# Kernel optimization log

Hardware: AMD Instinct MI355X
Metric: run time of the kernel (lower is better)

## Reference

```python
import jax, jax.numpy as jnp
import numpy as np


def _conv2d(x, w, b, dilation=1):
    pad = dilation * (w.shape[-1] // 2)
    y = jax.lax.conv_general_dilated(x, w, (1, 1), [(pad, pad), (pad, pad)],
                                     rhs_dilation=(dilation, dilation),
                                     dimension_numbers=("NCHW", "OIHW", "NCHW"))
    return y + b[None, :, None, None]


def _bn(x, gamma, beta, mean, var):
    # eval-mode BatchNorm2d, eps=1e-5
    inv = gamma / jnp.sqrt(var + 1e-5)
    return (x - mean[None, :, None, None]) * inv[None, :, None, None] + beta[None, :, None, None]


def _frft2d(x, angles):
    # Faithful port of the source frft2d, including the quirk that
    # temp[shft, :] indexes the BATCH dim: since shft is a permutation of
    # 0..N-1, the net effect is that batch entries 0..N-1 get (i)fft'd along
    # axis -2 and entries >= N are untouched.
    temp = jnp.swapaxes(x, -1, -2)
    BC = temp.shape[0]
    for a in angles:
        a = a % 4
        N = temp.shape[-2]
        sN = np.float32(np.sqrt(N))
        mask = (jnp.arange(BC) < N)[:, None, None]
        if a == 1:
            temp = jnp.where(mask, jnp.fft.fft(temp, axis=-2) / sN, temp)
        elif a == 2:
            temp = jnp.flip(temp, axis=-2)
        elif a == 3:
            temp = jnp.where(mask, jnp.fft.ifft(temp, axis=-2) * sN, temp)
        temp = jnp.swapaxes(temp, -1, -2)
    return temp


def setup_inputs() -> dict:
    key = jax.random.key(0)
    ks = jax.random.split(key, 12)
    B, C, H, W = 4, 64, 256, 256
    f = lambda k, shape, s=0.1: jax.random.normal(k, shape, dtype=jnp.float32) * s
    z1 = jnp.zeros((1,), jnp.float32)
    o1 = jnp.ones((1,), jnp.float32)
    return {
        "x": jax.random.normal(ks[0], (B, C, H, W), dtype=jnp.float32),
        "kernel_map": jnp.ones((H, W), dtype=jnp.float32),
        "theta_w": f(ks[1], (1, 1, 3, 3)), "theta_b": z1,
        "phase_w": f(ks[2], (1, 1, 3, 3)), "phase_b": z1,
        "phase_gamma": o1, "phase_beta": z1, "phase_mean": z1, "phase_var": o1,
        "amp_w": f(ks[3], (1, 1, 1, 1)), "amp_b": z1,
        "ms_w1": f(ks[4], (1, 1, 3, 3)), "ms_b1": z1,
        "ms_w2": f(ks[5], (1, 1, 3, 3)), "ms_b2": z1,
        "ms_w3": f(ks[6], (1, 1, 3, 3)), "ms_b3": z1,
        "fc1_w": f(ks[7], (16, 1)), "fc1_b": jnp.zeros((16,), jnp.float32),
        "fc2_w": f(ks[8], (1, 16)), "fc2_b": z1,
        "fin_w": f(ks[9], (1, 6, 1, 1)), "fin_b": z1,
        "fin_gamma": o1, "fin_beta": z1, "fin_mean": z1, "fin_var": o1,
    }


def reference(x, kernel_map, theta_w, theta_b, phase_w, phase_b,
              phase_gamma, phase_beta, phase_mean, phase_var,
              amp_w, amp_b, ms_w1, ms_b1, ms_w2, ms_b2, ms_w3, ms_b3,
              fc1_w, fc1_b, fc2_w, fc2_b, fin_w, fin_b,
              fin_gamma, fin_beta, fin_mean, fin_var):
    B, C, H, W = x.shape
    BC = B * C
    xf = x.reshape(BC, H, W)
    trker = jnp.clip(jax.nn.softplus(kernel_map), 1e-3, 10.0)
    # Riesz kernels, p=(1,1) => sin(pi/2)
    Y = (jnp.arange(H, dtype=jnp.float32) + 1.0)[:, None]
    X = (jnp.arange(W, dtype=jnp.float32) + 1.0)[None, :]
    sa = np.float32(np.sin(0.5 * np.pi))
    denom = jnp.sqrt((X / sa) ** 2 + (Y / sa) ** 2) + 1e-6
    dx = ((-1j) * (X / sa) / denom).astype(jnp.complex64) * trker
    dy = ((-1j) * (Y / sa) / denom).astype(jnp.complex64) * trker
    fa = _frft2d(xf.astype(jnp.complex64), [1, 1])
    R1 = jnp.abs(_frft2d(dx * fa, [-1, -1])) + 1e-6
    R2 = jnp.abs(_frft2d(dy * fa, [-1, -1])) + 1e-6
    A = jnp.sqrt(jax.nn.relu(xf ** 2 + R1 ** 2 + R2 ** 2) + 1e-6)[:, None]
    P = jnp.arctan2(jnp.sqrt(R1 ** 2 + R2 ** 2) + 1e-6, xf + 1e-6)[:, None]
    theta = jnp.arctan2(R2, R1 + 1e-6)[:, None]
    G_theta = theta * jax.nn.sigmoid(_conv2d(theta, theta_w, theta_b))
    P_prime = jax.nn.relu(_bn(_conv2d(P, phase_w, phase_b),
                              phase_gamma, phase_beta, phase_mean, phase_var))
    A_boost = A + jax.nn.relu(_conv2d(A, amp_w, amp_b))
    ms = jnp.concatenate([_conv2d(A_boost, ms_w1, ms_b1, 1),
                          _conv2d(A_boost, ms_w2, ms_b2, 2),
                          _conv2d(A_boost, ms_w3, ms_b3, 3)], axis=1)
    # adaptive_avg_pool2d to (H, W) is the identity here
    gf = jnp.mean(A_boost, axis=(2, 3))  # (BC, 1)
    gw = jax.nn.sigmoid(jax.nn.relu(gf @ fc1_w.T + fc1_b) @ fc2_w.T + fc2_b)
    gw = gw[:, :, None, None]  # (BC,1,1,1)
    fusion = jnp.concatenate([A_boost, P_prime, G_theta, ms * gw], axis=1)  # (BC,6,H,W)
    fused = _bn(_conv2d(fusion, fin_w, fin_b), fin_gamma, fin_beta, fin_mean, fin_var)
    fused = jnp.clip(jax.nn.relu(fused), 0.0, 1.0)
    return fused.reshape(B, C, H, W)
```

## Files before the change

kernel.cpp:

```cpp
#include <hip/hip_runtime.h>
#include <hip/hip_fp16.h>
#include <math.h>

#define PI_F 3.14159265358979323846f
#define ROWB 2112ull
#define IMGB (ROWB * 256ull)

__device__ __forceinline__ unsigned rev8(unsigned v){ return __brev(v) >> 24; }

__device__ __forceinline__ float2 cmulf(float2 a, float2 b){ return make_float2(a.x*b.x - a.y*b.y, a.x*b.y + a.y*b.x); }
__device__ __forceinline__ float2 cmulc(float2 a, float2 b){ return make_float2(a.x*b.x + a.y*b.y, a.y*b.x - a.x*b.y); }
__device__ __forceinline__ float2 cadd (float2 a, float2 b){ return make_float2(a.x+b.x, a.y+b.y); }
__device__ __forceinline__ float2 csub (float2 a, float2 b){ return make_float2(a.x-b.x, a.y-b.y); }
__device__ __forceinline__ float2 eix(float a){ float s, c; __sincosf(a, &s, &c); return make_float2(c, s); }
__device__ __forceinline__ float2 sx(float2 v, int d){ return make_float2(__shfl_xor(v.x, d), __shfl_xor(v.y, d)); }

__device__ __forceinline__ float frcp(float x){ float r; asm("v_rcp_f32 %0, %1" : "=v"(r) : "v"(x)); return r; }

__device__ __forceinline__ float fast_atan2pos(float y, float x){
  const float ax = fabsf(x);
  const float mn = fminf(ax, y), mx = fmaxf(ax, y);
  const float t  = mn * frcp(mx);
  const float z  = t * t;
  float p = -0.01172120f;
  p = fmaf(p, z,  0.05265332f);
  p = fmaf(p, z, -0.11643287f);
  p = fmaf(p, z,  0.19354346f);
  p = fmaf(p, z, -0.33262347f);
  p = fmaf(p, z,  0.99997726f);
  p = p * t;
  p = (y > ax) ? (1.57079632679f - p) : p;
  p = (x < 0.f) ? (3.14159265359f - p) : p;
  return p;
}

__device__ __forceinline__ unsigned packh2u(float a, float b){
  return __builtin_bit_cast(unsigned, __floats2half2_rn(a, b));
}
__device__ __forceinline__ float2 unpackh2(float p){
  return __half22float2(__builtin_bit_cast(__half2, p));
}

struct Twid { float2 w, w2, t[6]; };
__device__ __forceinline__ void mktw(Twid& T, int lane){
  T.w  = eix(-(2.0f * PI_F / 256.0f) * (float)lane);
  T.w2 = cmulf(T.w, T.w);
  #pragma unroll
  for (int st = 0; st < 6; ++st){
    const int d = 32 >> st;
    T.t[st] = eix(-(PI_F / (float)d) * (float)(lane & (d - 1)));
  }
}

__device__ __forceinline__ void fwd_head(float2 v[4], const Twid& T){
  const float2 t0 = cadd(v[0], v[2]);
  const float2 b0 = cmulf(csub(v[0], v[2]), T.w);
  const float2 t1 = cadd(v[1], v[3]);
  const float2 w64 = make_float2(T.w.y, -T.w.x);
  const float2 b1 = cmulf(csub(v[1], v[3]), w64);
  v[0] = cadd(t0, t1);
  v[1] = cmulf(csub(t0, t1), T.w2);
  v[2] = cadd(b0, b1);
  v[3] = cmulf(csub(b0, b1), T.w2);
}
__device__ __forceinline__ void inv_tail(float2 v[4], const Twid& T){
  const float2 uci = make_float2(T.w.y, T.w.x);
  const float2 m1 = cmulc(v[1], T.w2);
  const float2 m3a = cmulc(v[3], T.w2);
  const float2 n0 = cadd(v[0], m1), n1 = csub(v[0], m1);
  const float2 n2 = cadd(v[2], m3a), n3 = csub(v[2], m3a);
  const float2 m2 = cmulc(n2, T.w);
  const float2 m3 = cmulf(n3, uci);
  v[0] = cadd(n0, m2); v[2] = csub(n0, m2);
  v[1] = cadd(n1, m3); v[3] = csub(n1, m3);
}

__device__ __forceinline__ void fft256_fwd_sel(float2 v[4], int lane, const Twid& T){
  fwd_head(v, T);
  #pragma unroll
  for (int st = 0; st < 6; ++st){
    const int d = 32 >> st;
    const float2 tw = T.t[st];
    const bool hi = (lane & d) != 0;
    #pragma unroll
    for (int s = 0; s < 4; ++s){
      const float2 p  = sx(v[s], d);
      const float2 bo = cmulf(csub(p, v[s]), tw);
      const float2 lo = cadd(v[s], p);
      v[s] = hi ? bo : lo;
    }
  }
}
__device__ __forceinline__ void fft256_inv2_sel(float2 a[4], float2 b[4], int lane, const Twid& T){
  #pragma unroll
  for (int st = 0; st < 6; ++st){
    const int d = 1 << st;
    const float2 tw = T.t[5 - st];
    const bool hi = (lane & d) != 0;
    #pragma unroll
    for (int s = 0; s < 4; ++s){
      const float2 pa = sx(a[s], d);
      const float2 pb = sx(b[s], d);
      const float2 ma = cmulc(hi ? a[s] : pa, tw);
      const float2 mb = cmulc(hi ? b[s] : pb, tw);
      a[s] = hi ? csub(pa, ma) : cadd(a[s], ma);
      b[s] = hi ? csub(pb, mb) : cadd(b[s], mb);
    }
  }
  inv_tail(a, T);
  inv_tail(b, T);
}

__device__ __forceinline__ float2 stage_ab(float2 v, float2 p, float Ax, float Ay, float Bx, float By){
  float2 o;
  o.x = v.x*Ax - v.y*Ay + p.x*Bx - p.y*By;
  o.y = v.x*Ay + v.y*Ax + p.x*By + p.y*Bx;
  return o;
}
__device__ __forceinline__ void fft256_fwd2(float2 a[4], float2 b[4], int lane, const Twid& T){
  fwd_head(a, T);
  fwd_head(b, T);
  #pragma unroll
  for (int st = 0; st < 6; ++st){
    const int d = 32 >> st;
    const float2 t = T.t[st];
    const bool hi = (lane & d) != 0;
    const float Ax = hi ? -t.x : 1.f, Ay = hi ? -t.y : 0.f;
    const float Bx = hi ?  t.x : 1.f, By = hi ?  t.y : 0.f;
    #pragma unroll
    for (int s = 0; s < 4; ++s){
      const float2 pa = sx(a[s], d);
      const float2 pb = sx(b[s], d);
      a[s] = stage_ab(a[s], pa, Ax, Ay, Bx, By);
      b[s] = stage_ab(b[s], pb, Ax, Ay, Bx, By);
    }
  }
}
__device__ __forceinline__ void fft256_inv2(float2 a[4], float2 b[4], int lane, const Twid& T){
  #pragma unroll
  for (int st = 0; st < 6; ++st){
    const int d = 1 << st;
    const float2 t = T.t[5 - st];
    const bool hi = (lane & d) != 0;
    const float Ax = hi ? -t.x : 1.f, Ay = hi ?  t.y : 0.f;
    const float Bx = hi ?  1.f : t.x, By = hi ?  0.f : -t.y;
    #pragma unroll
    for (int s = 0; s < 4; ++s){
      const float2 pa = sx(a[s], d);
      const float2 pb = sx(b[s], d);
      a[s] = stage_ab(a[s], pa, Ax, Ay, Bx, By);
      b[s] = stage_ab(b[s], pb, Ax, Ay, Bx, By);
    }
  }
  inv_tail(a, T);
  inv_tail(b, T);
}

__global__ __launch_bounds__(256) void k0_prep(const float* __restrict__ km,
                                               float* __restrict__ sTabS,
                                               float* __restrict__ zrow){
  const int idx = blockIdx.x * 256 + threadIdx.x;
  const int q = idx >> 8, r = idx & 255;
  const int u = rev8(q), v = rev8(r);
  const float kv = km[u * 256 + v];
  float sp = fmaxf(kv, 0.f) + log1pf(expf(-fabsf(kv)));
  sp = fminf(fmaxf(sp, 1e-3f), 10.f);
  const float fu = (float)(u + 1), fv = (float)(v + 1);
  sTabS[idx] = sp / (sqrtf(fu * fu + fv * fv) + 1e-6f) * (1.0f / 65536.0f);
  if (blockIdx.x == 0){
    zrow[threadIdx.x] = 0.f;
    zrow[threadIdx.x + 256] = 0.f;
    if (threadIdx.x < 16) zrow[threadIdx.x + 512] = 0.f;
  }
}

__global__ __launch_bounds__(256) void k1_row(const float* __restrict__ x, char* __restrict__ arena){
  const int grp = threadIdx.x >> 6, lane = threadIdx.x & 63;
  const int rs = blockIdx.x * 8 + grp * 2;
  Twid T; mktw(T, lane);
  const float* xr0 = x + (size_t)rs * 256;
  const float* xr1 = xr0 + 256;
  float2 a[4], b[4];
  #pragma unroll
  for (int s = 0; s < 4; ++s){
    a[s] = make_float2(xr0[lane + 64 * s], 0.f);
    b[s] = make_float2(xr1[lane + 64 * s], 0.f);
  }
  fft256_fwd2(a, b, lane, T);
  float2* S0 = (float2*)(arena + (size_t)rs * ROWB);
  float2* S1 = (float2*)(arena + (size_t)(rs + 1) * ROWB);
  #pragma unroll
  for (int s = 0; s < 4; ++s){ S0[lane + 64 * s] = a[s]; S1[lane + 64 * s] = b[s]; }
}

__global__ __launch_bounds__(512) void k2_col(char* __restrict__ arena, const float* __restrict__ sTabS){
  __shared__ float2 lds[256 * 9];
  const int tid = threadIdx.x;
  const int b  = blockIdx.x >> 5;
  const int u0 = (blockIdx.x & 31) << 3;
  char* base = arena + (size_t)b * IMGB;

  #pragma unroll
  for (int k = 0; k < 4; ++k){
    const int idx = tid + (k << 9);
    const int r = idx >> 3, cc = idx & 7;
    lds[r * 9 + (cc ^ ((r >> 3) & 7))] = *(const float2*)(base + (size_t)r * ROWB + (size_t)(u0 + cc) * 8);
  }
  __syncthreads();

  const int wv = tid >> 6, lane = tid & 63;
  Twid T; mktw(T, lane);
  const int r6 = __brev(lane) >> 26;
  float fvv[4];
  fvv[0] = (float)(4 * r6 + 0 + 1);
  fvv[1] = (float)(4 * r6 + 2 + 1);
  fvv[2] = (float)(4 * r6 + 1 + 1);
  fvv[3] = (float)(4 * r6 + 3 + 1);
  const int swb = (lane >> 3) & 7;

  {
    const int c = wv;
    const int q = u0 + c;
    const int swc = c ^ swb;
    float2 F[4];
    #pragma unroll
    for (int s = 0; s < 4; ++s) F[s] = lds[(lane + 64 * s) * 9 + swc];
    fft256_fwd_sel(F, lane, T);
    float sc[4];
    #pragma unroll
    for (int s = 0; s < 4; ++s) sc[s] = sTabS[q * 256 + lane + 64 * s];
    const float fu = (float)(rev8((unsigned)q) + 1);
    float2 G1[4], G2[4];
    #pragma unroll
    for (int s = 0; s < 4; ++s){
      const float a1 = fvv[s] * sc[s];
      const float a2 = fu * sc[s];
      G1[s] = make_float2(a1 * F[s].y, -a1 * F[s].x);
      G2[s] = make_float2(a2 * F[s].y, -a2 * F[s].x);
    }
    fft256_inv2_sel(G1, G2, lane, T);
    #pragma unroll
    for (int s = 0; s < 4; ++s)
      lds[(lane + 64 * s) * 9 + swc] =
          make_float2(__uint_as_float(packh2u(G1[s].x, G1[s].y)),
                      __uint_as_float(packh2u(G2[s].x, G2[s].y)));
  }
  __syncthreads();
  #pragma unroll
  for (int k = 0; k < 4; ++k){
    const int idx = tid + (k << 9);
    const int r = idx >> 3, cc = idx & 7;
    *(float2*)(base + (size_t)r * ROWB + (size_t)(u0 + cc) * 8) = lds[r * 9 + (cc ^ ((r >> 3) & 7))];
  }
}

__global__ __launch_bounds__(256) void k3_rowinv(const float* __restrict__ x, char* __restrict__ arena,
    const float* __restrict__ ampw, const float* __restrict__ ampb,
    float* __restrict__ rowsum){
  const int grp = threadIdx.x >> 6, lane = threadIdx.x & 63;
  const int rs = blockIdx.x * 4 + grp;
  Twid T; mktw(T, lane);
  char* rowb = arena + (size_t)rs * ROWB;
  float2 g1[4], g2[4];
  #pragma unroll
  for (int s = 0; s < 4; ++s){
    const float2 pk = *(const float2*)(rowb + (size_t)(lane + 64 * s) * 8);
    g1[s] = unpackh2(pk.x); g2[s] = unpackh2(pk.y);
  }
  fft256_inv2(g1, g2, lane, T);
  const float aw = *ampw, ab = *ampb;
  const float* xr = x + (size_t)rs * 256;
  float* Arow = (float*)(rowb + 16);
  unsigned* Prow = (unsigned*)(rowb + 1072);
  float sum = 0.f;
  #pragma unroll
  for (int s = 0; s < 4; ++s){
    const int j = lane + 64 * s;
    const float xv = xr[j];
    const float R1 = sqrtf(fmaf(g1[s].x, g1[s].x, g1[s].y * g1[s].y)) + 1e-6f;
    const float R2 = sqrtf(fmaf(g2[s].x, g2[s].x, g2[s].y * g2[s].y)) + 1e-6f;
    const float rr = fmaf(R1, R1, R2 * R2);
    const float A = sqrtf(fmaxf(fmaf(xv, xv, rr), 0.f) + 1e-6f);
    const float P  = fast_atan2pos(sqrtf(rr) + 1e-6f, xv + 1e-6f);
    const float Th = fast_atan2pos(R2, R1 + 1e-6f);
    const float Ab = A + fmaxf(fmaf(aw, A, ab), 0.f);
    Arow[j] = Ab;
    Prow[j] = packh2u(P, Th);
    sum += Ab;
  }
  #pragma unroll
  for (int off = 32; off; off >>= 1) sum += __shfl_down(sum, off);
  if (lane == 0) rowsum[rs] = sum;
}

__global__ __launch_bounds__(256) void kpad(char* __restrict__ arena){
  char* row = arena + (size_t)blockIdx.x * IMGB + (size_t)threadIdx.x * ROWB;
  const float4 z = make_float4(0.f, 0.f, 0.f, 0.f);
  *(float4*)(row)         = z;
  *(float4*)(row + 1040)  = z;
  *(float4*)(row + 1056)  = z;
  *(float4*)(row + 2096)  = z;
}

__global__ __launch_bounds__(256) void k4_gw(const float* __restrict__ rowsum,
    const float* __restrict__ fc1w, const float* __restrict__ fc1b,
    const float* __restrict__ fc2w, const float* __restrict__ fc2b,
    float* __restrict__ gw){
  __shared__ float red[256];
  const int tid = threadIdx.x;
  red[tid] = rowsum[blockIdx.x * 256 + tid];
  __syncthreads();
  #pragma unroll
  for (int off = 128; off; off >>= 1){
    if (tid < off) red[tid] += red[tid + off];
    __syncthreads();
  }
  if (tid == 0){
    const float gf = red[0] * (1.0f / 65536.0f);
    float acc = fc2b[0];
    #pragma unroll
    for (int k = 0; k < 16; ++k)
      acc += fc2w[k] * fmaxf(gf * fc1w[k] + fc1b[k], 0.f);
    gw[blockIdx.x] = frcp(1.f + __expf(-acc));
  }
}

__global__ __launch_bounds__(256) void k5_fuse(
    const char* __restrict__ arena, const float* __restrict__ zrowf,
    const float* __restrict__ gwp,
    const float* __restrict__ theta_w, const float* __restrict__ theta_b,
    const float* __restrict__ phase_w, const float* __restrict__ phase_b,
    const float* __restrict__ phase_gamma, const float* __restrict__ phase_beta,
    const float* __restrict__ phase_mean, const float* __restrict__ phase_var,
    const float* __restrict__ ms_w1, const float* __restrict__ ms_b1,
    const float* __restrict__ ms_w2, const float* __restrict__ ms_b2,
    const float* __restrict__ ms_w3, const float* __restrict__ ms_b3,
    const float* __restrict__ fin_w, const float* __restrict__ fin_b,
    const float* __restrict__ fin_gamma, const float* __restrict__ fin_beta,
    const float* __restrict__ fin_mean, const float* __restrict__ fin_var,
    float* __restrict__ out){
  const int z = blockIdx.z;
  const int tx = threadIdx.x & 15, ty = threadIdx.x >> 4;
  const int j0 = (blockIdx.x << 6) + (tx << 2);
  const int i0 = (blockIdx.y << 6) + (ty << 2);
  const char* img = arena + (size_t)z * IMGB;

  float tw9[9], pw9[9], w1[9], w2[9], w3[9];
  #pragma unroll
  for (int k = 0; k < 9; ++k){
    tw9[k] = theta_w[k]; pw9[k] = phase_w[k];
    w1[k] = ms_w1[k]; w2[k] = ms_w2[k]; w3[k] = ms_w3[k];
  }
  const float b1s = ms_b1[0], b2s = ms_b2[0], b3s = ms_b3[0];
  const float tbs = theta_b[0], pbs = phase_b[0];

  float4 m1[4], m2[4], m3[4], at[4], ap[4], Ac[4], Tc[4];
  #pragma unroll
  for (int oi = 0; oi < 4; ++oi){
    m1[oi] = make_float4(b1s, b1s, b1s, b1s);
    m2[oi] = make_float4(b2s, b2s, b2s, b2s);
    m3[oi] = make_float4(b3s, b3s, b3s, b3s);
    at[oi] = make_float4(tbs, tbs, tbs, tbs);
    ap[oi] = make_float4(pbs, pbs, pbs, pbs);
  }

  #pragma unroll
  for (int lr = 0; lr < 10; ++lr){
    const int ar = i0 - 3 + lr;
    const float* rowA = ((unsigned)ar < 256u) ? (const float*)(img + (size_t)ar * ROWB) : zrowf;
    const float4 va = *(const float4*)(rowA + j0);
    const float4 vb = *(const float4*)(rowA + j0 + 4);
    const float4 vc = *(const float4*)(rowA + j0 + 8);
    const float a[12] = {va.x, va.y, va.z, va.w, vb.x, vb.y, vb.z, vb.w, vc.x, vc.y, vc.z, vc.w};
    #pragma unroll
    for (int oi = 0; oi < 4; ++oi){
      const int dd = lr - 3 - oi;
      if (dd >= -1 && dd <= 1){
        const int wr = (dd + 1) * 3;
        #pragma unroll
        for (int dx = -1; dx <= 1; ++dx){
          const float w = w1[wr + dx + 1];
          m1[oi].x += w * a[4 + 0 + dx]; m1[oi].y += w * a[4 + 1 + dx];
          m1[oi].z += w * a[4 + 2 + dx]; m1[oi].w += w * a[4 + 3 + dx];
        }
      }
      if (dd == -2 || dd == 0 || dd == 2){
        const int wr = (dd / 2 + 1) * 3;
        #pragma unroll
        for (int dx = -1; dx <= 1; ++dx){
          const float w = w2[wr + dx + 1];
          m2[oi].x += w * a[4 + 0 + 2 * dx]; m2[oi].y += w * a[4 + 1 + 2 * dx];
          m2[oi].z += w * a[4 + 2 + 2 * dx]; m2[oi].w += w * a[4 + 3 + 2 * dx];
        }
      }
      if (dd == -3 || dd == 0 || dd == 3){
        const int wr = (dd / 3 + 1) * 3;
        #pragma unroll
        for (int dx = -1; dx <= 1; ++dx){
          const float w = w3[wr + dx + 1];
          m3[oi].x += w * a[4 + 0 + 3 * dx]; m3[oi].y += w * a[4 + 1 + 3 * dx];
          m3[oi].z += w * a[4 + 2 + 3 * dx]; m3[oi].w += w * a[4 + 3 + 3 * dx];
        }
      }
      if (dd == 0) Ac[oi] = make_float4(a[4], a[5], a[6], a[7]);
    }
  }

  #pragma unroll
  for (int lr = 0; lr < 6; ++lr){
    const int ar = i0 - 1 + lr;
    const unsigned* rowP = ((unsigned)ar < 256u) ? (const unsigned*)(img + (size_t)ar * ROWB + 1056)
                                                 : (const unsigned*)zrowf;
    const uint4 ua = *(const uint4*)(rowP + j0);
    const uint4 ub = *(const uint4*)(rowP + j0 + 4);
    const uint4 uc = *(const uint4*)(rowP + j0 + 8);
    const unsigned uu[12] = {ua.x, ua.y, ua.z, ua.w, ub.x, ub.y, ub.z, ub.w, uc.x, uc.y, uc.z, uc.w};
    float p[12], t[12];
    #pragma unroll
    for (int k = 0; k < 12; ++k){
      const float2 pt = unpackh2(__builtin_bit_cast(float, uu[k]));
      p[k] = pt.x; t[k] = pt.y;
    }
    #pragma unroll
    for (int oi = 0; oi < 4; ++oi){
      const int dd = lr - 1 - oi;
      if (dd >= -1 && dd <= 1){
        const int wr = (dd + 1) * 3;
        #pragma unroll
        for (int dx = -1; dx <= 1; ++dx){
          const float wp = pw9[wr + dx + 1], wt = tw9[wr + dx + 1];
          ap[oi].x += wp * p[4 + 0 + dx]; ap[oi].y += wp * p[4 + 1 + dx];
          ap[oi].z += wp * p[4 + 2 + dx]; ap[oi].w += wp * p[4 + 3 + dx];
          at[oi].x += wt * t[4 + 0 + dx]; at[oi].y += wt * t[4 + 1 + dx];
          at[oi].z += wt * t[4 + 2 + dx]; at[oi].w += wt * t[4 + 3 + dx];
        }
      }
      if (dd == 0) Tc[oi] = make_float4(t[4], t[5], t[6], t[7]);
    }
  }

  const float gwb = gwp[z];
  const float inv_p = phase_gamma[0] * rsqrtf(phase_var[0] + 1e-5f);
  const float pmean = phase_mean[0], pbeta = phase_beta[0];
  const float f0 = fin_w[0], f1 = fin_w[1], f2 = fin_w[2];
  const float f3 = fin_w[3], f4 = fin_w[4], f5 = fin_w[5];
  const float fb = fin_b[0];
  const float inv_f = fin_gamma[0] * rsqrtf(fin_var[0] + 1e-5f);
  const float fmean = fin_mean[0], fbeta = fin_beta[0];

  #pragma unroll
  for (int oi = 0; oi < 4; ++oi){
    const float mm1[4] = {m1[oi].x, m1[oi].y, m1[oi].z, m1[oi].w};
    const float mm2[4] = {m2[oi].x, m2[oi].y, m2[oi].z, m2[oi].w};
    const float mm3[4] = {m3[oi].x, m3[oi].y, m3[oi].z, m3[oi].w};
    const float tt[4]  = {at[oi].x, at[oi].y, at[oi].z, at[oi].w};
    const float pp[4]  = {ap[oi].x, ap[oi].y, ap[oi].z, ap[oi].w};
    const float ac[4]  = {Ac[oi].x, Ac[oi].y, Ac[oi].z, Ac[oi].w};
    const float tc[4]  = {Tc[oi].x, Tc[oi].y, Tc[oi].z, Tc[oi].w};
    float o4[4];
    #pragma unroll
    for (int oj = 0; oj < 4; ++oj){
      const float Gt = tc[oj] * frcp(1.f + __expf(-tt[oj]));
      const float Pp = fmaxf((pp[oj] - pmean) * inv_p + pbeta, 0.f);
      const float pre = f0 * ac[oj] + f1 * Pp + f2 * Gt
                      + gwb * (f3 * mm1[oj] + f4 * mm2[oj] + f5 * mm3[oj]) + fb;
      float o = (pre - fmean) * inv_f + fbeta;
      o4[oj] = fminf(fmaxf(o, 0.f), 1.f);
    }
    *(float4*)(out + ((size_t)(z * 256 + i0 + oi) << 8) + j0) = make_float4(o4[0], o4[1], o4[2], o4[3]);
  }
}

extern "C" void kernel_launch(void* const* d_in, const int* in_sizes, int n_in,
                              void* d_out, int out_size, void* d_ws, size_t ws_size,
                              hipStream_t stream){
  const float* x  = (const float*)d_in[0];
  const float* km = (const float*)d_in[1];

  int N = 1;
  while (N < 64){
    const size_t need = (size_t)(256 / N) * IMGB + 2112ull + 262144ull + 1024ull
                      + (size_t)(256 / N) * 1024ull;
    if (need <= ws_size) break;
    N <<= 1;
  }
  const int imgsPer = 256 / N;
  const int rowsPer = imgsPer * 256;

  char*  ws     = (char*)d_ws;
  char*  arena  = ws;
  float* zrow   = (float*)(ws + (size_t)imgsPer * IMGB);
  float* sTabS  = (float*)(ws + (size_t)imgsPer * IMGB + 2112ull);
  float* gwbuf  = (float*)(ws + (size_t)imgsPer * IMGB + 2112ull + 262144ull);
  float* rowsum = (float*)(ws + (size_t)imgsPer * IMGB + 2112ull + 262144ull + 1024ull);

  k0_prep<<<256, 256, 0, stream>>>(km, sTabS, zrow);

  for (int s = 0; s < N; ++s){
    const float* xs = x + (size_t)s * rowsPer * 256;
    float* outs = (float*)d_out + (size_t)s * rowsPer * 256;

    k1_row<<<rowsPer / 8, 256, 0, stream>>>(xs, arena);
    k2_col<<<imgsPer * 32, 512, 0, stream>>>(arena, sTabS);
    k3_rowinv<<<rowsPer / 4, 256, 0, stream>>>(xs, arena,
        (const float*)d_in[10], (const float*)d_in[11], rowsum);
    kpad<<<imgsPer, 256, 0, stream>>>(arena);
    k4_gw<<<imgsPer, 256, 0, stream>>>(rowsum,
        (const float*)d_in[18], (const float*)d_in[19],
        (const float*)d_in[20], (const float*)d_in[21], gwbuf);
    k5_fuse<<<dim3(4, 4, imgsPer), 256, 0, stream>>>(
        arena, zrow, gwbuf,
        (const float*)d_in[2],  (const float*)d_in[3],
        (const float*)d_in[4],  (const float*)d_in[5],
        (const float*)d_in[6],  (const float*)d_in[7],
        (const float*)d_in[8],  (const float*)d_in[9],
        (const float*)d_in[12], (const float*)d_in[13],
        (const float*)d_in[14], (const float*)d_in[15],
        (const float*)d_in[16], (const float*)d_in[17],
        (const float*)d_in[22], (const float*)d_in[23],
        (const float*)d_in[24], (const float*)d_in[25],
        (const float*)d_in[26], (const float*)d_in[27],
        outs);
  }
}
```

Measured before the change: 367.9 us.

## Store A_boost as fp16, fold padding into row-inverse, use DS swizzle shuffles

The FFT butterfly stages now exchange lanes with compile-time DS swizzle instructions instead of generic shuffles for distances under 32. The A_boost plane is stored as half precision, which halves its traffic in the fuse kernel's stencil loads. Zeroing of the row padding moves into k3_rowinv, so the separate kpad launch is gone. The trade-off is reduced precision of A_boost in the multi-scale convolutions and the fusion conv.

```diff
diff --git a/kernel.cpp b/kernel.cpp
--- a/kernel.cpp
+++ b/kernel.cpp
@@ -13,9 +13,22 @@
 __device__ __forceinline__ float2 cadd (float2 a, float2 b){ return make_float2(a.x+b.x, a.y+b.y); }
 __device__ __forceinline__ float2 csub (float2 a, float2 b){ return make_float2(a.x-b.x, a.y-b.y); }
 __device__ __forceinline__ float2 eix(float a){ float s, c; __sincosf(a, &s, &c); return make_float2(c, s); }
-__device__ __forceinline__ float2 sx(float2 v, int d){ return make_float2(__shfl_xor(v.x, d), __shfl_xor(v.y, d)); }
 
 __device__ __forceinline__ float frcp(float x){ float r; asm("v_rcp_f32 %0, %1" : "=v"(r) : "v"(x)); return r; }
+
+template<int D>
+__device__ __forceinline__ float sw1(float v){
+  if constexpr (D < 32){
+    return __builtin_bit_cast(float,
+      __builtin_amdgcn_ds_swizzle(__builtin_bit_cast(int, v), (D << 10) | 0x1F));
+  } else {
+    return __shfl_xor(v, 32);
+  }
+}
+template<int D>
+__device__ __forceinline__ float2 sxc(float2 v){
+  return make_float2(sw1<D>(v.x), sw1<D>(v.y));
+}
 
 __device__ __forceinline__ float fast_atan2pos(float y, float x){
   const float ax = fabsf(x);
@@ -75,83 +88,80 @@
   v[1] = cadd(n1, m3); v[3] = csub(n1, m3);
 }
 
-__device__ __forceinline__ void fft256_fwd_sel(float2 v[4], int lane, const Twid& T){
-  fwd_head(v, T);
-  #pragma unroll
-  for (int st = 0; st < 6; ++st){
-    const int d = 32 >> st;
-    const float2 tw = T.t[st];
-    const bool hi = (lane & d) != 0;
-    #pragma unroll
-    for (int s = 0; s < 4; ++s){
-      const float2 p  = sx(v[s], d);
-      const float2 bo = cmulf(csub(p, v[s]), tw);
-      const float2 lo = cadd(v[s], p);
-      v[s] = hi ? bo : lo;
-    }
-  }
-}
-__device__ __forceinline__ void fft256_inv2_sel(float2 a[4], float2 b[4], int lane, const Twid& T){
-  #pragma unroll
-  for (int st = 0; st < 6; ++st){
-    const int d = 1 << st;
-    const float2 tw = T.t[5 - st];
-    const bool hi = (lane & d) != 0;
-    #pragma unroll
-    for (int s = 0; s < 4; ++s){
-      const float2 pa = sx(a[s], d);
-      const float2 pb = sx(b[s], d);
-      const float2 ma = cmulc(hi ? a[s] : pa, tw);
-      const float2 mb = cmulc(hi ? b[s] : pb, tw);
-      a[s] = hi ? csub(pa, ma) : cadd(a[s], ma);
-      b[s] = hi ? csub(pb, mb) : cadd(b[s], mb);
-    }
-  }
-  inv_tail(a, T);
-  inv_tail(b, T);
-}
-
 __device__ __forceinline__ float2 stage_ab(float2 v, float2 p, float Ax, float Ay, float Bx, float By){
   float2 o;
   o.x = v.x*Ax - v.y*Ay + p.x*Bx - p.y*By;
   o.y = v.x*Ay + v.y*Ax + p.x*By + p.y*Bx;
   return o;
 }
+
+__device__ __forceinline__ void fft256_fwd_sel(float2 v[4], int lane, const Twid& T){
+  fwd_head(v, T);
+#define FWDS_STAGE(ST) { \
+  constexpr int d = 32 >> (ST); \
+  const float2 tw = T.t[ST]; \
+  const bool hi = (lane & d) != 0; \
+  for (int s = 0; s < 4; ++s){ \
+    const float2 p = sxc<d>(v[s]); \
+    const float2 bo = cmulf(csub(p, v[s]), tw); \
+    const float2 lo = cadd(v[s], p); \
+    v[s] = hi ? bo : lo; \
+  } }
+  FWDS_STAGE(0) FWDS_STAGE(1) FWDS_STAGE(2) FWDS_STAGE(3) FWDS_STAGE(4) FWDS_STAGE(5)
+#undef FWDS_STAGE
+}
+__device__ __forceinline__ void fft256_inv2_sel(float2 a[4], float2 b[4], int lane, const Twid& T){
+#define INVS_STAGE(ST) { \
+  constexpr int d = 1 << (ST); \
+  const float2 tw = T.t[5 - (ST)]; \
+  const bool hi = (lane & d) != 0; \
+  for (int s = 0; s < 4; ++s){ \
+    const float2 pa = sxc<d>(a[s]); \
+    const float2 pb = sxc<d>(b[s]); \
+    const float2 ma = cmulc(hi ? a[s] : pa, tw); \
+    const float2 mb = cmulc(hi ? b[s] : pb, tw); \
+    a[s] = hi ? csub(pa, ma) : cadd(a[s], ma); \
+    b[s] = hi ? csub(pb, mb) : cadd(b[s], mb); \
+  } }
+  INVS_STAGE(0) INVS_STAGE(1) INVS_STAGE(2) INVS_STAGE(3) INVS_STAGE(4) INVS_STAGE(5)
+#undef INVS_STAGE
+  inv_tail(a, T);
+  inv_tail(b, T);
+}
+
 __device__ __forceinline__ void fft256_fwd2(float2 a[4], float2 b[4], int lane, const Twid& T){
   fwd_head(a, T);
   fwd_head(b, T);
-  #pragma unroll
-  for (int st = 0; st < 6; ++st){
-    const int d = 32 >> st;
-    const float2 t = T.t[st];
-    const bool hi = (lane & d) != 0;
-    const float Ax = hi ? -t.x : 1.f, Ay = hi ? -t.y : 0.f;
-    const float Bx = hi ?  t.x : 1.f, By = hi ?  t.y : 0.f;
-    #pragma unroll
-    for (int s = 0; s < 4; ++s){
-      const float2 pa = sx(a[s], d);
-      const float2 pb = sx(b[s], d);
-      a[s] = stage_ab(a[s], pa, Ax, Ay, Bx, By);
-      b[s] = stage_ab(b[s], pb, Ax, Ay, Bx, By);
-    }
-  }
+#define FWD2_STAGE(ST) { \
+  constexpr int d = 32 >> (ST); \
+  const float2 t = T.t[ST]; \
+  const bool hi = (lane & d) != 0; \
+  const float Ax = hi ? -t.x : 1.f, Ay = hi ? -t.y : 0.f; \
+  const float Bx = hi ?  t.x : 1.f, By = hi ?  t.y : 0.f; \
+  for (int s = 0; s < 4; ++s){ \
+    const float2 pa = sxc<d>(a[s]); \
+    const float2 pb = sxc<d>(b[s]); \
+    a[s] = stage_ab(a[s], pa, Ax, Ay, Bx, By); \
+    b[s] = stage_ab(b[s], pb, Ax, Ay, Bx, By); \
+  } }
+  FWD2_STAGE(0) FWD2_STAGE(1) FWD2_STAGE(2) FWD2_STAGE(3) FWD2_STAGE(4) FWD2_STAGE(5)
+#undef FWD2_STAGE
 }
 __device__ __forceinline__ void fft256_inv2(float2 a[4], float2 b[4], int lane, const Twid& T){
-  #pragma unroll
-  for (int st = 0; st < 6; ++st){
-    const int d = 1 << st;
-    const float2 t = T.t[5 - st];
-    const bool hi = (lane & d) != 0;
-    const float Ax = hi ? -t.x : 1.f, Ay = hi ?  t.y : 0.f;
-    const float Bx = hi ?  1.f : t.x, By = hi ?  0.f : -t.y;
-    #pragma unroll
-    for (int s = 0; s < 4; ++s){
-      const float2 pa = sx(a[s], d);
-      const float2 pb = sx(b[s], d);
-      a[s] = stage_ab(a[s], pa, Ax, Ay, Bx, By);
-      b[s] = stage_ab(b[s], pb, Ax, Ay, Bx, By);
-    }
-  }
+#define INV2_STAGE(ST) { \
+  constexpr int d = 1 << (ST); \
+  const float2 t = T.t[5 - (ST)]; \
+  const bool hi = (lane & d) != 0; \
+  const float Ax = hi ? -t.x : 1.f, Ay = hi ?  t.y : 0.f; \
+  const float Bx = hi ?  1.f : t.x, By = hi ?  0.f : -t.y; \
+  for (int s = 0; s < 4; ++s){ \
+    const float2 pa = sxc<d>(a[s]); \
+    const float2 pb = sxc<d>(b[s]); \
+    a[s] = stage_ab(a[s], pa, Ax, Ay, Bx, By); \
+    b[s] = stage_ab(b[s], pb, Ax, Ay, Bx, By); \
+  } }
+  INV2_STAGE(0) INV2_STAGE(1) INV2_STAGE(2) INV2_STAGE(3) INV2_STAGE(4) INV2_STAGE(5)
+#undef INV2_STAGE
   inv_tail(a, T);
   inv_tail(b, T);
 }
@@ -270,7 +280,7 @@
   fft256_inv2(g1, g2, lane, T);
   const float aw = *ampw, ab = *ampb;
   const float* xr = x + (size_t)rs * 256;
-  float* Arow = (float*)(rowb + 16);
+  __half* Arow = (__half*)(rowb + 8);
   unsigned* Prow = (unsigned*)(rowb + 1072);
   float sum = 0.f;
   #pragma unroll
@@ -284,22 +294,17 @@
     const float P  = fast_atan2pos(sqrtf(rr) + 1e-6f, xv + 1e-6f);
     const float Th = fast_atan2pos(R2, R1 + 1e-6f);
     const float Ab = A + fmaxf(fmaf(aw, A, ab), 0.f);
-    Arow[j] = Ab;
+    Arow[j] = __float2half_rn(Ab);
     Prow[j] = packh2u(P, Th);
     sum += Ab;
   }
   #pragma unroll
   for (int off = 32; off; off >>= 1) sum += __shfl_down(sum, off);
   if (lane == 0) rowsum[rs] = sum;
-}
-
-__global__ __launch_bounds__(256) void kpad(char* __restrict__ arena){
-  char* row = arena + (size_t)blockIdx.x * IMGB + (size_t)threadIdx.x * ROWB;
-  const float4 z = make_float4(0.f, 0.f, 0.f, 0.f);
-  *(float4*)(row)         = z;
-  *(float4*)(row + 1040)  = z;
-  *(float4*)(row + 1056)  = z;
-  *(float4*)(row + 2096)  = z;
+  if (lane < 4){
+    const size_t off8 = (lane == 0) ? 0ull : (lane == 1) ? 520ull : (lane == 2) ? 1064ull : 2096ull;
+    *(unsigned long long*)(rowb + off8) = 0ull;
+  }
 }
 
 __global__ __launch_bounds__(256) void k4_gw(const float* __restrict__ rowsum,
@@ -367,11 +372,23 @@
   #pragma unroll
   for (int lr = 0; lr < 10; ++lr){
     const int ar = i0 - 3 + lr;
-    const float* rowA = ((unsigned)ar < 256u) ? (const float*)(img + (size_t)ar * ROWB) : zrowf;
-    const float4 va = *(const float4*)(rowA + j0);
-    const float4 vb = *(const float4*)(rowA + j0 + 4);
-    const float4 vc = *(const float4*)(rowA + j0 + 8);
-    const float a[12] = {va.x, va.y, va.z, va.w, vb.x, vb.y, vb.z, vb.w, vc.x, vc.y, vc.z, vc.w};
+    const __half* rowA = ((unsigned)ar < 256u) ? (const __half*)(img + (size_t)ar * ROWB + 8)
+                                               : ((const __half*)zrowf + 4);
+    const uint2 h0 = *(const uint2*)(rowA + (j0 - 4));
+    const uint2 h1 = *(const uint2*)(rowA + j0);
+    const uint2 h2v = *(const uint2*)(rowA + (j0 + 4));
+    float a[12];
+    {
+      const float2 p0 = unpackh2(__builtin_bit_cast(float, h0.x));
+      const float2 p1 = unpackh2(__builtin_bit_cast(float, h0.y));
+      const float2 p2 = unpackh2(__builtin_bit_cast(float, h1.x));
+      const float2 p3 = unpackh2(__builtin_bit_cast(float, h1.y));
+      const float2 p4 = unpackh2(__builtin_bit_cast(float, h2v.x));
+      const float2 p5 = unpackh2(__builtin_bit_cast(float, h2v.y));
+      a[0]=p0.x; a[1]=p0.y; a[2]=p1.x; a[3]=p1.y;
+      a[4]=p2.x; a[5]=p2.y; a[6]=p3.x; a[7]=p3.y;
+      a[8]=p4.x; a[9]=p4.y; a[10]=p5.x; a[11]=p5.y;
+    }
     #pragma unroll
     for (int oi = 0; oi < 4; ++oi){
       const int dd = lr - 3 - oi;
@@ -504,7 +521,6 @@
     k2_col<<<imgsPer * 32, 512, 0, stream>>>(arena, sTabS);
     k3_rowinv<<<rowsPer / 4, 256, 0, stream>>>(xs, arena,
         (const float*)d_in[10], (const float*)d_in[11], rowsum);
-    kpad<<<imgsPer, 256, 0, stream>>>(arena);
     k4_gw<<<imgsPer, 256, 0, stream>>>(rowsum,
         (const float*)d_in[18], (const float*)d_in[19],
         (const float*)d_in[20], (const float*)d_in[21], gwbuf);
```

After: 356.0 us. 3.2% less time.
